# Kernel tuning notes

Hardware: AMD Instinct MI355X
Metric: run time of the kernel (lower is better)

## Reference

```python
import jax, jax.numpy as jnp
import numpy as np

N_NODES = 100000
N_EDGES = 600000
IN_C = 128


def setup_inputs() -> dict:
    key = jax.random.key(0)
    ks = jax.random.split(key, 10)
    x = jax.random.normal(ks[0], (N_NODES, IN_C), dtype=jnp.float32)
    edge_index = jax.random.randint(ks[1], (2, N_EDGES), 0, N_NODES, dtype=jnp.int64)
    edge_weight = jax.random.uniform(ks[2], (N_EDGES,), dtype=jnp.float32)
    s = 1.0 / np.sqrt(IN_C)
    # EvolveGCNO initial GCN weight [in, in]
    W0 = jax.random.uniform(ks[3], (IN_C, IN_C), minval=-s, maxval=s, dtype=jnp.float32)
    # GRU(input=in, hidden=in) params, gate order (r, z, n)
    W_ih = jax.random.uniform(ks[4], (3 * IN_C, IN_C), minval=-s, maxval=s, dtype=jnp.float32)
    W_hh = jax.random.uniform(ks[5], (3 * IN_C, IN_C), minval=-s, maxval=s, dtype=jnp.float32)
    b_ih = jax.random.uniform(ks[6], (3 * IN_C,), minval=-s, maxval=s, dtype=jnp.float32)
    b_hh = jax.random.uniform(ks[7], (3 * IN_C,), minval=-s, maxval=s, dtype=jnp.float32)
    cls_w = jax.random.uniform(ks[8], (1, IN_C), minval=-s, maxval=s, dtype=jnp.float32)
    cls_b = jax.random.uniform(ks[9], (1,), minval=-s, maxval=s, dtype=jnp.float32)
    return {"x": x, "edge_index": edge_index, "edge_weight": edge_weight,
            "W0": W0, "W_ih": W_ih, "W_hh": W_hh, "b_ih": b_ih, "b_hh": b_hh,
            "cls_w": cls_w, "cls_b": cls_b}


def reference(x, edge_index, edge_weight, W0, W_ih, W_hh, b_ih, b_hh, cls_w, cls_b):
    n = x.shape[0]
    # --- EvolveGCNO: GRU step with input = hidden = W0 (batch = in_channels rows) ---
    gi = W0 @ W_ih.T + b_ih
    gh = W0 @ W_hh.T + b_hh
    i_r, i_z, i_n = jnp.split(gi, 3, axis=1)
    h_r, h_z, h_n = jnp.split(gh, 3, axis=1)
    r = jax.nn.sigmoid(i_r + h_r)
    z = jax.nn.sigmoid(i_z + h_z)
    cand = jnp.tanh(i_n + r * h_n)
    W = (1.0 - z) * cand + z * W0  # evolved GCN weight [in, in]
    # --- GCNConv with fixed W: add self-loops, symmetric normalization ---
    loops = jnp.arange(n, dtype=edge_index.dtype)
    row = jnp.concatenate([edge_index[0], loops])  # source
    col = jnp.concatenate([edge_index[1], loops])  # target
    w = jnp.concatenate([edge_weight, jnp.ones((n,), x.dtype)])
    deg = jax.ops.segment_sum(w, col, num_segments=n)
    dinv = jnp.where(deg > 0, jax.lax.rsqrt(jnp.maximum(deg, 1e-30)), 0.0)
    norm = dinv[row] * w * dinv[col]  # [E+N]
    h = x @ W  # [N, in]
    agg = jax.ops.segment_sum(norm[:, None] * h[row], col, num_segments=n)  # [N, in]
    # --- ReLU + linear classifier ---
    h = jax.nn.relu(agg)
    return h @ cls_w.T + cls_b  # [N, 1]
```

## Files before the change

kernel.cpp:

```cpp
#include <hip/hip_runtime.h>
#include <math.h>

#define IN_C 128
#define CAP 32
#define CAP_LO 8
#define CAP_HI 24

typedef short short8 __attribute__((ext_vector_type(8)));
typedef float floatx4 __attribute__((ext_vector_type(4)));
typedef unsigned long long u64;

static __device__ __forceinline__ unsigned short f2bf(float f) {
    unsigned int u = __float_as_uint(f);
    u += 0x7fffu + ((u >> 16) & 1u);
    return (unsigned short)(u >> 16);
}

static __device__ __forceinline__ float bflo(unsigned int v) { return __uint_as_float(v << 16); }
static __device__ __forceinline__ float bfhi(unsigned int v) { return __uint_as_float(v & 0xffff0000u); }

__global__ __launch_bounds__(256) void zero_evolve(
        const float* __restrict__ W0, const float* __restrict__ Wih,
        const float* __restrict__ Whh, const float* __restrict__ bih,
        const float* __restrict__ bhh, unsigned short* __restrict__ Wbt,
        u64* __restrict__ pk, int n, int ZB) {
    const int b = blockIdx.x;
    const int t = threadIdx.x;
    if (b < 64) {
        __shared__ float w0row[2][IN_C];
        const int r2 = t >> 7;
        const int j = t & 127;
        const int i = b * 2 + r2;
        w0row[r2][j] = W0[i * IN_C + j];
        __syncthreads();
        float ir = bih[j], iz = bih[j + IN_C], inn = bih[j + 2 * IN_C];
        float hr = bhh[j], hz = bhh[j + IN_C], hnn = bhh[j + 2 * IN_C];
        const float* wr = &Wih[(size_t)j * IN_C];
        const float* wz = &Wih[(size_t)(j + IN_C) * IN_C];
        const float* wn = &Wih[(size_t)(j + 2 * IN_C) * IN_C];
        const float* ur = &Whh[(size_t)j * IN_C];
        const float* uz = &Whh[(size_t)(j + IN_C) * IN_C];
        const float* un = &Whh[(size_t)(j + 2 * IN_C) * IN_C];
        #pragma unroll 4
        for (int k = 0; k < IN_C; ++k) {
            const float a = w0row[r2][k];
            ir = fmaf(a, wr[k], ir); iz = fmaf(a, wz[k], iz); inn = fmaf(a, wn[k], inn);
            hr = fmaf(a, ur[k], hr); hz = fmaf(a, uz[k], hz); hnn = fmaf(a, un[k], hnn);
        }
        const float r = 1.0f / (1.0f + expf(-(ir + hr)));
        const float z = 1.0f / (1.0f + expf(-(iz + hz)));
        const float cand = tanhf(inn + r * hnn);
        Wbt[j * IN_C + i] = f2bf((1.0f - z) * cand + z * w0row[r2][j]);
    } else {
        uint4* z = (uint4*)pk;
        const size_t nquad = ((size_t)n * (CAP_LO + 1)) >> 1;
        const uint4 zero4 = make_uint4(0u, 0u, 0u, 0u);
        const size_t stride = (size_t)ZB * 256;
        for (size_t i = (size_t)(b - 64) * 256 + t; i < nquad; i += stride) z[i] = zero4;
    }
}

#define ALD 136
__global__ __launch_bounds__(256) void hist_place_gemm(
        const int* __restrict__ rowi, const int* __restrict__ coli,
        const float* __restrict__ ew,
        u64* __restrict__ pk, u64* __restrict__ cap_lo, u64* __restrict__ cap_hi,
        int E, int EB, int M,
        const float* __restrict__ x, const unsigned short* __restrict__ Wbt,
        unsigned short* __restrict__ hb, int n) {
    __shared__ unsigned short As[128 * ALD];
    __shared__ unsigned short Ws[128 * ALD];
    const int i = blockIdx.x;
    const int t = threadIdx.x;
    const int prev = (int)(((long long)i * EB) / M);
    const int next = (int)(((long long)(i + 1) * EB) / M);

    if (next > prev) {
        const int e0 = (prev * 256 + t) * 4;
        int eBeg = e0, eEnd = (e0 + 4 <= E) ? e0 + 4 : E;
        if (e0 + 3 < E) {
            const int4 r4 = *(const int4*)&rowi[e0];
            const int4 c4 = *(const int4*)&coli[e0];
            const float4 w4 = *(const float4*)&ew[e0];
            const int rr[4] = {r4.x, r4.y, r4.z, r4.w};
            const int cc[4] = {c4.x, c4.y, c4.z, c4.w};
            const float ww[4] = {w4.x, w4.y, w4.z, w4.w};
            u64 old[4];
            #pragma unroll
            for (int k = 0; k < 4; ++k)
                old[k] = atomicAdd(&pk[cc[k]], (1ull << 32) | (u64)(unsigned int)(ww[k] * 16777216.0f));
            #pragma unroll
            for (int k = 0; k < 4; ++k) {
                const unsigned int rk = (unsigned int)(old[k] >> 32);
                const u64 val = (u64)(unsigned)rr[k] | ((u64)__float_as_uint(ww[k]) << 32);
                if (rk < CAP_LO)
                    __builtin_nontemporal_store(val, &cap_lo[(size_t)cc[k] * CAP_LO + rk]);
                else if (rk < CAP)
                    __builtin_nontemporal_store(val, &cap_hi[(size_t)cc[k] * CAP_HI + (rk - CAP_LO)]);
            }
        } else {
            for (int e = eBeg; e < eEnd; ++e) {
                const u64 o = atomicAdd(&pk[coli[e]],
                    (1ull << 32) | (u64)(unsigned int)(ew[e] * 16777216.0f));
                const unsigned int rk = (unsigned int)(o >> 32);
                const u64 val = (u64)(unsigned)rowi[e] | ((u64)__float_as_uint(ew[e]) << 32);
                if (rk < CAP_LO) cap_lo[(size_t)coli[e] * CAP_LO + rk] = val;
                else if (rk < CAP) cap_hi[(size_t)coli[e] * CAP_HI + (rk - CAP_LO)] = val;
            }
        }
        return;
    }

    const size_t row0 = (size_t)(i - prev) * 128;

    for (int idx = t; idx < 2048; idx += 256) {
        const int nn = idx >> 4, k8 = (idx & 15) * 8;
        *(uint4*)&Ws[nn * ALD + k8] = *(const uint4*)&Wbt[nn * IN_C + k8];
    }
    for (int idx = t; idx < 4096; idx += 256) {
        const int r = idx >> 5, c4 = (idx & 31) * 4;
        size_t row = row0 + r;
        if (row >= (size_t)n) row = (size_t)n - 1;
        const float4 v = *(const float4*)&x[row * IN_C + c4];
        ushort4 bb;
        bb.x = f2bf(v.x); bb.y = f2bf(v.y); bb.z = f2bf(v.z); bb.w = f2bf(v.w);
        *(ushort4*)&As[r * ALD + c4] = bb;
    }
    __syncthreads();

    const int w = t >> 6, lane = t & 63, ln = lane & 15, quad = lane >> 4;
    floatx4 acc[2][8];
    #pragma unroll
    for (int mt = 0; mt < 2; ++mt)
        #pragma unroll
        for (int nt = 0; nt < 8; ++nt)
            acc[mt][nt] = (floatx4){0.f, 0.f, 0.f, 0.f};

    #pragma unroll
    for (int k0 = 0; k0 < 128; k0 += 32) {
        const short8 a0 = *(const short8*)&As[(w * 32 + ln) * ALD + k0 + quad * 8];
        const short8 a1 = *(const short8*)&As[(w * 32 + 16 + ln) * ALD + k0 + quad * 8];
        #pragma unroll
        for (int nt = 0; nt < 8; ++nt) {
            const short8 bb = *(const short8*)&Ws[(nt * 16 + ln) * ALD + k0 + quad * 8];
            acc[0][nt] = __builtin_amdgcn_mfma_f32_16x16x32_bf16(a0, bb, acc[0][nt], 0, 0, 0);
            acc[1][nt] = __builtin_amdgcn_mfma_f32_16x16x32_bf16(a1, bb, acc[1][nt], 0, 0, 0);
        }
    }

    #pragma unroll
    for (int mt = 0; mt < 2; ++mt) {
        #pragma unroll
        for (int reg = 0; reg < 4; ++reg) {
            const size_t row = row0 + w * 32 + mt * 16 + quad * 4 + reg;
            if (row < (size_t)n) {
                #pragma unroll
                for (int nt = 0; nt < 8; ++nt)
                    hb[row * IN_C + nt * 16 + ln] = f2bf(acc[mt][nt][reg]);
            }
        }
    }
}

__global__ __launch_bounds__(256) void gather_classify(
        const unsigned short* __restrict__ hb, const u64* __restrict__ pk,
        const u64* __restrict__ cap_lo, const u64* __restrict__ cap_hi,
        const float* __restrict__ cls_w, const float* __restrict__ cls_b,
        float* __restrict__ out, int n) {
    const int gwid = (blockIdx.x * blockDim.x + threadIdx.x) >> 6;
    const int lane = threadIdx.x & 63;
    const int sub = lane >> 4;
    const int sl = lane & 15;
    const int nid = gwid * 4 + sub;
    if (nid >= n) return;

    const int ch0 = sl * 8;

    const u64 pv = pk[nid];
    const uint4 hs = *(const uint4*)&hb[(size_t)nid * IN_C + ch0];
    u64 p[8];
    #pragma unroll
    for (int i = 0; i < 8; ++i) p[i] = cap_lo[(size_t)nid * CAP_LO + i];

    float s0 = 0.f, s1 = 0.f, s2 = 0.f, s3 = 0.f, s4 = 0.f, s5 = 0.f, s6 = 0.f, s7 = 0.f;

    {
        u64 q[8];
        uint4 hr[8];
        #pragma unroll
        for (int i = 0; i < 8; ++i) {
            const unsigned int src = (unsigned int)p[i];
            q[i] = pk[src];
            hr[i] = *(const uint4*)&hb[(size_t)src * IN_C + ch0];
        }
        #pragma unroll
        for (int i = 0; i < 8; ++i) {
            const float w = __uint_as_float((unsigned int)(p[i] >> 32));
            const float dvs = rsqrtf((float)(unsigned int)q[i] * (1.0f / 16777216.0f) + 1.0f);
            const float nm = w * dvs;
            s0 = fmaf(nm, bflo(hr[i].x), s0); s1 = fmaf(nm, bfhi(hr[i].x), s1);
            s2 = fmaf(nm, bflo(hr[i].y), s2); s3 = fmaf(nm, bfhi(hr[i].y), s3);
            s4 = fmaf(nm, bflo(hr[i].z), s4); s5 = fmaf(nm, bfhi(hr[i].z), s5);
            s6 = fmaf(nm, bflo(hr[i].w), s6); s7 = fmaf(nm, bfhi(hr[i].w), s7);
        }
    }

    int cnt = (int)(pv >> 32);
    if (cnt > CAP) cnt = CAP;
    for (int e = CAP_LO; e < cnt; e += 8) {
        u64 p2[8];
        #pragma unroll
        for (int i = 0; i < 8; ++i) {
            const int idx = (e + i < cnt) ? (e + i) : (cnt - 1);
            p2[i] = cap_hi[(size_t)nid * CAP_HI + (idx - CAP_LO)];
        }
        u64 q[8];
        uint4 hr[8];
        #pragma unroll
        for (int i = 0; i < 8; ++i) {
            const unsigned int src = (unsigned int)p2[i];
            q[i] = pk[src];
            hr[i] = *(const uint4*)&hb[(size_t)src * IN_C + ch0];
        }
        #pragma unroll
        for (int i = 0; i < 8; ++i) {
            const float w = __uint_as_float((unsigned int)(p2[i] >> 32));
            const float dvs = rsqrtf((float)(unsigned int)q[i] * (1.0f / 16777216.0f) + 1.0f);
            const float nm = (e + i < cnt) ? w * dvs : 0.0f;
            s0 = fmaf(nm, bflo(hr[i].x), s0); s1 = fmaf(nm, bfhi(hr[i].x), s1);
            s2 = fmaf(nm, bflo(hr[i].y), s2); s3 = fmaf(nm, bfhi(hr[i].y), s3);
            s4 = fmaf(nm, bflo(hr[i].z), s4); s5 = fmaf(nm, bfhi(hr[i].z), s5);
            s6 = fmaf(nm, bflo(hr[i].w), s6); s7 = fmaf(nm, bfhi(hr[i].w), s7);
        }
    }

    const float dvc = rsqrtf((float)(unsigned int)pv * (1.0f / 16777216.0f) + 1.0f);
    const float4 wva = *(const float4*)&cls_w[ch0];
    const float4 wvb = *(const float4*)&cls_w[ch0 + 4];
    float sum =
        wva.x * fmaxf(dvc * fmaf(dvc, bflo(hs.x), s0), 0.f) +
        wva.y * fmaxf(dvc * fmaf(dvc, bfhi(hs.x), s1), 0.f) +
        wva.z * fmaxf(dvc * fmaf(dvc, bflo(hs.y), s2), 0.f) +
        wva.w * fmaxf(dvc * fmaf(dvc, bfhi(hs.y), s3), 0.f) +
        wvb.x * fmaxf(dvc * fmaf(dvc, bflo(hs.z), s4), 0.f) +
        wvb.y * fmaxf(dvc * fmaf(dvc, bfhi(hs.z), s5), 0.f) +
        wvb.z * fmaxf(dvc * fmaf(dvc, bflo(hs.w), s6), 0.f) +
        wvb.w * fmaxf(dvc * fmaf(dvc, bfhi(hs.w), s7), 0.f);
    #pragma unroll
    for (int off = 8; off > 0; off >>= 1) sum += __shfl_down(sum, off, 16);
    if (sl == 0) out[nid] = sum + cls_b[0];
}

extern "C" void kernel_launch(void* const* d_in, const int* in_sizes, int n_in,
                              void* d_out, int out_size, void* d_ws, size_t ws_size,
                              hipStream_t stream) {
    const float* x    = (const float*)d_in[0];
    const int*   eidx = (const int*)d_in[1];
    const float* ew   = (const float*)d_in[2];
    const float* W0   = (const float*)d_in[3];
    const float* Wih  = (const float*)d_in[4];
    const float* Whh  = (const float*)d_in[5];
    const float* bih  = (const float*)d_in[6];
    const float* bhh  = (const float*)d_in[7];
    const float* clsw = (const float*)d_in[8];
    const float* clsb = (const float*)d_in[9];
    float* out = (float*)d_out;

    const int n = in_sizes[0] / IN_C;
    const int E = in_sizes[2];
    const int* rowi = eidx;
    const int* coli = eidx + E;

    u64* pk = (u64*)d_ws;
    u64* cap_lo = pk + n;
    u64* cap_hi = cap_lo + (size_t)n * CAP_LO;
    unsigned short* Wbt = (unsigned short*)(cap_hi + (size_t)n * CAP_HI);
    unsigned short* hb  = Wbt + 16384;

    const int EB = (E + 1023) / 1024;
    const int GB = (n + 127) / 128;
    const int M = EB + GB;
    const int ZB = 256;

    zero_evolve<<<dim3(64 + ZB), dim3(256), 0, stream>>>(W0, Wih, Whh, bih, bhh, Wbt, pk, n, ZB);
    hist_place_gemm<<<dim3(M), dim3(256), 0, stream>>>(rowi, coli, ew, pk, cap_lo, cap_hi,
                                                       E, EB, M, x, Wbt, hb, n);
    const int waves = (n + 3) / 4;
    gather_classify<<<dim3((waves + 3) / 4), dim3(256), 0, stream>>>(hb, pk, cap_lo, cap_hi,
                                                                     clsw, clsb, out, n);
}
```

Baseline: 193.7 us.

## Skip zeroing the edge slot buffer and use eight lanes per node in gather

The zero pass now clears only the per-node packed counter array, not the cap_lo slot buffer. Unfilled slots in the first eight are instead handled in the gather by clamping the source index and masking the weight by the edge count. The gather now gives each node 8 lanes with 16 channels each instead of 16 lanes with 8 channels, and batches neighbours four at a time, so more nodes are in flight per wave. The cost is more registers per lane and reads of possibly stale slot data that must be masked correctly.

```diff
diff --git a/kernel.cpp b/kernel.cpp
--- a/kernel.cpp
+++ b/kernel.cpp
@@ -53,7 +53,7 @@
         Wbt[j * IN_C + i] = f2bf((1.0f - z) * cand + z * w0row[r2][j]);
     } else {
         uint4* z = (uint4*)pk;
-        const size_t nquad = ((size_t)n * (CAP_LO + 1)) >> 1;
+        const size_t nquad = (size_t)n >> 1;
         const uint4 zero4 = make_uint4(0u, 0u, 0u, 0u);
         const size_t stride = (size_t)ZB * 256;
         for (size_t i = (size_t)(b - 64) * 256 + t; i < nquad; i += stride) z[i] = zero4;
@@ -77,7 +77,6 @@
 
     if (next > prev) {
         const int e0 = (prev * 256 + t) * 4;
-        int eBeg = e0, eEnd = (e0 + 4 <= E) ? e0 + 4 : E;
         if (e0 + 3 < E) {
             const int4 r4 = *(const int4*)&rowi[e0];
             const int4 c4 = *(const int4*)&coli[e0];
@@ -99,7 +98,7 @@
                     __builtin_nontemporal_store(val, &cap_hi[(size_t)cc[k] * CAP_HI + (rk - CAP_LO)]);
             }
         } else {
-            for (int e = eBeg; e < eEnd; ++e) {
+            for (int e = e0; e < E; ++e) {
                 const u64 o = atomicAdd(&pk[coli[e]],
                     (1ull << 32) | (u64)(unsigned int)(ew[e] * 16777216.0f));
                 const unsigned int rk = (unsigned int)(o >> 32);
@@ -169,85 +168,113 @@
         float* __restrict__ out, int n) {
     const int gwid = (blockIdx.x * blockDim.x + threadIdx.x) >> 6;
     const int lane = threadIdx.x & 63;
-    const int sub = lane >> 4;
-    const int sl = lane & 15;
-    const int nid = gwid * 4 + sub;
+    const int sub = lane >> 3;
+    const int sl = lane & 7;
+    const int nid = gwid * 8 + sub;
     if (nid >= n) return;
 
-    const int ch0 = sl * 8;
+    const int ch0 = sl * 16;
+    const unsigned int un = (unsigned int)n;
 
     const u64 pv = pk[nid];
-    const uint4 hs = *(const uint4*)&hb[(size_t)nid * IN_C + ch0];
+    const uint4 hsA = *(const uint4*)&hb[(size_t)nid * IN_C + ch0];
+    const uint4 hsB = *(const uint4*)&hb[(size_t)nid * IN_C + ch0 + 8];
     u64 p[8];
     #pragma unroll
     for (int i = 0; i < 8; ++i) p[i] = cap_lo[(size_t)nid * CAP_LO + i];
 
-    float s0 = 0.f, s1 = 0.f, s2 = 0.f, s3 = 0.f, s4 = 0.f, s5 = 0.f, s6 = 0.f, s7 = 0.f;
-
-    {
-        u64 q[8];
-        uint4 hr[8];
-        #pragma unroll
-        for (int i = 0; i < 8; ++i) {
-            const unsigned int src = (unsigned int)p[i];
-            q[i] = pk[src];
-            hr[i] = *(const uint4*)&hb[(size_t)src * IN_C + ch0];
-        }
-        #pragma unroll
-        for (int i = 0; i < 8; ++i) {
-            const float w = __uint_as_float((unsigned int)(p[i] >> 32));
-            const float dvs = rsqrtf((float)(unsigned int)q[i] * (1.0f / 16777216.0f) + 1.0f);
-            const float nm = w * dvs;
-            s0 = fmaf(nm, bflo(hr[i].x), s0); s1 = fmaf(nm, bfhi(hr[i].x), s1);
-            s2 = fmaf(nm, bflo(hr[i].y), s2); s3 = fmaf(nm, bfhi(hr[i].y), s3);
-            s4 = fmaf(nm, bflo(hr[i].z), s4); s5 = fmaf(nm, bfhi(hr[i].z), s5);
-            s6 = fmaf(nm, bflo(hr[i].w), s6); s7 = fmaf(nm, bfhi(hr[i].w), s7);
-        }
-    }
+    float s[16];
+    #pragma unroll
+    for (int i = 0; i < 16; ++i) s[i] = 0.f;
 
     int cnt = (int)(pv >> 32);
     if (cnt > CAP) cnt = CAP;
-    for (int e = CAP_LO; e < cnt; e += 8) {
-        u64 p2[8];
-        #pragma unroll
-        for (int i = 0; i < 8; ++i) {
+
+    #pragma unroll
+    for (int bb = 0; bb < 2; ++bb) {
+        u64 q[4];
+        uint4 hrA[4], hrB[4];
+        #pragma unroll
+        for (int i = 0; i < 4; ++i) {
+            unsigned int src = (unsigned int)p[bb * 4 + i];
+            src = (src < un) ? src : (un - 1);
+            q[i] = pk[src];
+            hrA[i] = *(const uint4*)&hb[(size_t)src * IN_C + ch0];
+            hrB[i] = *(const uint4*)&hb[(size_t)src * IN_C + ch0 + 8];
+        }
+        #pragma unroll
+        for (int i = 0; i < 4; ++i) {
+            const float w = __uint_as_float((unsigned int)(p[bb * 4 + i] >> 32));
+            const float dvs = rsqrtf((float)(unsigned int)q[i] * (1.0f / 16777216.0f) + 1.0f);
+            const float nm = (bb * 4 + i < cnt) ? w * dvs : 0.0f;
+            s[0]  = fmaf(nm, bflo(hrA[i].x), s[0]);  s[1]  = fmaf(nm, bfhi(hrA[i].x), s[1]);
+            s[2]  = fmaf(nm, bflo(hrA[i].y), s[2]);  s[3]  = fmaf(nm, bfhi(hrA[i].y), s[3]);
+            s[4]  = fmaf(nm, bflo(hrA[i].z), s[4]);  s[5]  = fmaf(nm, bfhi(hrA[i].z), s[5]);
+            s[6]  = fmaf(nm, bflo(hrA[i].w), s[6]);  s[7]  = fmaf(nm, bfhi(hrA[i].w), s[7]);
+            s[8]  = fmaf(nm, bflo(hrB[i].x), s[8]);  s[9]  = fmaf(nm, bfhi(hrB[i].x), s[9]);
+            s[10] = fmaf(nm, bflo(hrB[i].y), s[10]); s[11] = fmaf(nm, bfhi(hrB[i].y), s[11]);
+            s[12] = fmaf(nm, bflo(hrB[i].z), s[12]); s[13] = fmaf(nm, bfhi(hrB[i].z), s[13]);
+            s[14] = fmaf(nm, bflo(hrB[i].w), s[14]); s[15] = fmaf(nm, bfhi(hrB[i].w), s[15]);
+        }
+    }
+
+    for (int e = CAP_LO; e < cnt; e += 4) {
+        u64 p2[4];
+        #pragma unroll
+        for (int i = 0; i < 4; ++i) {
             const int idx = (e + i < cnt) ? (e + i) : (cnt - 1);
             p2[i] = cap_hi[(size_t)nid * CAP_HI + (idx - CAP_LO)];
         }
-        u64 q[8];
-        uint4 hr[8];
-        #pragma unroll
-        for (int i = 0; i < 8; ++i) {
+        u64 q[4];
+        uint4 hrA[4], hrB[4];
+        #pragma unroll
+        for (int i = 0; i < 4; ++i) {
             const unsigned int src = (unsigned int)p2[i];
             q[i] = pk[src];
-            hr[i] = *(const uint4*)&hb[(size_t)src * IN_C + ch0];
-        }
-        #pragma unroll
-        for (int i = 0; i < 8; ++i) {
+            hrA[i] = *(const uint4*)&hb[(size_t)src * IN_C + ch0];
+            hrB[i] = *(const uint4*)&hb[(size_t)src * IN_C + ch0 + 8];
+        }
+        #pragma unroll
+        for (int i = 0; i < 4; ++i) {
             const float w = __uint_as_float((unsigned int)(p2[i] >> 32));
             const float dvs = rsqrtf((float)(unsigned int)q[i] * (1.0f / 16777216.0f) + 1.0f);
             const float nm = (e + i < cnt) ? w * dvs : 0.0f;
-            s0 = fmaf(nm, bflo(hr[i].x), s0); s1 = fmaf(nm, bfhi(hr[i].x), s1);
-            s2 = fmaf(nm, bflo(hr[i].y), s2); s3 = fmaf(nm, bfhi(hr[i].y), s3);
-            s4 = fmaf(nm, bflo(hr[i].z), s4); s5 = fmaf(nm, bfhi(hr[i].z), s5);
-            s6 = fmaf(nm, bflo(hr[i].w), s6); s7 = fmaf(nm, bfhi(hr[i].w), s7);
+            s[0]  = fmaf(nm, bflo(hrA[i].x), s[0]);  s[1]  = fmaf(nm, bfhi(hrA[i].x), s[1]);
+            s[2]  = fmaf(nm, bflo(hrA[i].y), s[2]);  s[3]  = fmaf(nm, bfhi(hrA[i].y), s[3]);
+            s[4]  = fmaf(nm, bflo(hrA[i].z), s[4]);  s[5]  = fmaf(nm, bfhi(hrA[i].z), s[5]);
+            s[6]  = fmaf(nm, bflo(hrA[i].w), s[6]);  s[7]  = fmaf(nm, bfhi(hrA[i].w), s[7]);
+            s[8]  = fmaf(nm, bflo(hrB[i].x), s[8]);  s[9]  = fmaf(nm, bfhi(hrB[i].x), s[9]);
+            s[10] = fmaf(nm, bflo(hrB[i].y), s[10]); s[11] = fmaf(nm, bfhi(hrB[i].y), s[11]);
+            s[12] = fmaf(nm, bflo(hrB[i].z), s[12]); s[13] = fmaf(nm, bfhi(hrB[i].z), s[13]);
+            s[14] = fmaf(nm, bflo(hrB[i].w), s[14]); s[15] = fmaf(nm, bfhi(hrB[i].w), s[15]);
         }
     }
 
     const float dvc = rsqrtf((float)(unsigned int)pv * (1.0f / 16777216.0f) + 1.0f);
-    const float4 wva = *(const float4*)&cls_w[ch0];
-    const float4 wvb = *(const float4*)&cls_w[ch0 + 4];
+    const float4 wv0 = *(const float4*)&cls_w[ch0];
+    const float4 wv1 = *(const float4*)&cls_w[ch0 + 4];
+    const float4 wv2 = *(const float4*)&cls_w[ch0 + 8];
+    const float4 wv3 = *(const float4*)&cls_w[ch0 + 12];
     float sum =
-        wva.x * fmaxf(dvc * fmaf(dvc, bflo(hs.x), s0), 0.f) +
-        wva.y * fmaxf(dvc * fmaf(dvc, bfhi(hs.x), s1), 0.f) +
-        wva.z * fmaxf(dvc * fmaf(dvc, bflo(hs.y), s2), 0.f) +
-        wva.w * fmaxf(dvc * fmaf(dvc, bfhi(hs.y), s3), 0.f) +
-        wvb.x * fmaxf(dvc * fmaf(dvc, bflo(hs.z), s4), 0.f) +
-        wvb.y * fmaxf(dvc * fmaf(dvc, bfhi(hs.z), s5), 0.f) +
-        wvb.z * fmaxf(dvc * fmaf(dvc, bflo(hs.w), s6), 0.f) +
-        wvb.w * fmaxf(dvc * fmaf(dvc, bfhi(hs.w), s7), 0.f);
-    #pragma unroll
-    for (int off = 8; off > 0; off >>= 1) sum += __shfl_down(sum, off, 16);
+        wv0.x * fmaxf(dvc * fmaf(dvc, bflo(hsA.x), s[0]), 0.f) +
+        wv0.y * fmaxf(dvc * fmaf(dvc, bfhi(hsA.x), s[1]), 0.f) +
+        wv0.z * fmaxf(dvc * fmaf(dvc, bflo(hsA.y), s[2]), 0.f) +
+        wv0.w * fmaxf(dvc * fmaf(dvc, bfhi(hsA.y), s[3]), 0.f) +
+        wv1.x * fmaxf(dvc * fmaf(dvc, bflo(hsA.z), s[4]), 0.f) +
+        wv1.y * fmaxf(dvc * fmaf(dvc, bfhi(hsA.z), s[5]), 0.f) +
+        wv1.z * fmaxf(dvc * fmaf(dvc, bflo(hsA.w), s[6]), 0.f) +
+        wv1.w * fmaxf(dvc * fmaf(dvc, bfhi(hsA.w), s[7]), 0.f) +
+        wv2.x * fmaxf(dvc * fmaf(dvc, bflo(hsB.x), s[8]), 0.f) +
+        wv2.y * fmaxf(dvc * fmaf(dvc, bfhi(hsB.x), s[9]), 0.f) +
+        wv2.z * fmaxf(dvc * fmaf(dvc, bflo(hsB.y), s[10]), 0.f) +
+        wv2.w * fmaxf(dvc * fmaf(dvc, bfhi(hsB.y), s[11]), 0.f) +
+        wv3.x * fmaxf(dvc * fmaf(dvc, bflo(hsB.z), s[12]), 0.f) +
+        wv3.y * fmaxf(dvc * fmaf(dvc, bfhi(hsB.z), s[13]), 0.f) +
+        wv3.z * fmaxf(dvc * fmaf(dvc, bflo(hsB.w), s[14]), 0.f) +
+        wv3.w * fmaxf(dvc * fmaf(dvc, bfhi(hsB.w), s[15]), 0.f);
+    sum += __shfl_down(sum, 4, 8);
+    sum += __shfl_down(sum, 2, 8);
+    sum += __shfl_down(sum, 1, 8);
     if (sl == 0) out[nid] = sum + cls_b[0];
 }
 
@@ -280,12 +307,12 @@
     const int EB = (E + 1023) / 1024;
     const int GB = (n + 127) / 128;
     const int M = EB + GB;
-    const int ZB = 256;
+    const int ZB = 64;
 
     zero_evolve<<<dim3(64 + ZB), dim3(256), 0, stream>>>(W0, Wih, Whh, bih, bhh, Wbt, pk, n, ZB);
     hist_place_gemm<<<dim3(M), dim3(256), 0, stream>>>(rowi, coli, ew, pk, cap_lo, cap_hi,
                                                        E, EB, M, x, Wbt, hb, n);
-    const int waves = (n + 3) / 4;
+    const int waves = (n + 7) / 8;
     gather_classify<<<dim3((waves + 3) / 4), dim3(256), 0, stream>>>(hb, pk, cap_lo, cap_hi,
                                                                      clsw, clsb, out, n);
 }
```

Result: no change. 191.3 us (median of 2 runs) (-1.3%).
